# Optimization experiments

Hardware: AMD Instinct MI355X
Metric: run time of the kernel (lower is better)

Reference implementation:

```python
import jax, jax.numpy as jnp
import numpy as np

_BLOCK = 32          # _QUANTIZATION_BLOCK_SIZE
_UPPER = 8           # upper_bound = 2**(4-1)-1 + 1 for Q4_0 (bitwidth=4)
_QMAX = 15.0         # 2**bitwidth - 1


def _q4_0_dequant(kernel):
    """Vectorized Q4_0 fake-quantization over 32-element blocks (last axis, no transpose)."""
    orig_dtype = kernel.dtype
    nb = kernel.size // _BLOCK
    blocks = kernel.reshape(nb, _BLOCK).astype(jnp.float32)  # [nb, 32]
    # signed value at the abs-argmax position of each block
    amax_idx = jnp.argmax(jnp.abs(blocks), axis=1)
    max_val = jnp.take_along_axis(blocks, amax_idx[:, None], axis=1)  # [nb, 1]
    d = -max_val / _UPPER
    safe_d = jnp.where(d == 0.0, 1.0, d)
    safe_inv_d = jnp.where(d == 0.0, 0.0, 1.0 / safe_d)
    scale = d.astype(jnp.float16).astype(jnp.float32)  # fp16 scale round-trip
    qs = jnp.clip(jnp.trunc(blocks * safe_inv_d + (_UPPER + 0.5)), 0.0, _QMAX)
    deq = scale * (qs - _UPPER)
    return deq.reshape(kernel.shape).astype(orig_dtype)


def _ste_q4_0(kernel):
    """Straight-through estimator wrapper (identity gradient)."""
    zero = kernel - jax.lax.stop_gradient(kernel)
    return zero + jax.lax.stop_gradient(_q4_0_dequant(kernel))


def setup_inputs() -> dict:
    key = jax.random.key(0)
    k1, k2, k3 = jax.random.split(key, 3)
    d_in, features = 8192, 8192
    inputs = jax.random.normal(k1, (1, 32, d_in), dtype=jnp.float32)
    kernel = jax.random.normal(k2, (d_in, features), dtype=jnp.float32) * 0.02
    bias = jax.random.normal(k3, (features,), dtype=jnp.float32) * 0.02
    return {"inputs": inputs, "kernel": kernel, "bias": bias}


def reference(inputs, kernel, bias):
    w = _ste_q4_0(kernel)                      # fake-quantized weight [d_in, features]
    y = inputs @ w                             # [B, S, features]
    y = y + bias
    return y
```

## Files before the change

### kernel.cpp

```cpp
#include <hip/hip_runtime.h>
#include <hip/hip_fp16.h>

#define MDIM 32
#define KDIM 8192
#define NDIM 8192
#define NT 128
#define KC 512
#define BK 64
#define NTILES (KC / BK)
#define WSTRIDE 72

typedef __fp16 half8 __attribute__((ext_vector_type(8)));
typedef float f32x4 __attribute__((ext_vector_type(4)));

__device__ __forceinline__ unsigned pk_u32(float a, float b) {
#if __has_builtin(__builtin_amdgcn_cvt_pkrtz)
  return __builtin_bit_cast(unsigned, __builtin_amdgcn_cvt_pkrtz(a, b));
#else
  __fp16 r2[2] = {(__fp16)a, (__fp16)b};
  return __builtin_bit_cast(unsigned, r2);
#endif
}

__global__ __launch_bounds__(256) void xpack_kernel(const float* __restrict__ x,
                                                    uint4* __restrict__ xpf) {
  const int T  = blockIdx.x * 256 + threadIdx.x;
  const int sg = T >> 7;
  const int r  = T & 127;
  const int mt = r >> 6;
  const int L  = r & 63;
  const int m  = mt * 16 + (L & 15);
  const int k  = sg * 32 + (L >> 4) * 8;
  const float4* p = reinterpret_cast<const float4*>(x + (size_t)m * KDIM + k);
  float4 u0 = p[0], u1 = p[1];
  uint4 o;
  o.x = pk_u32(u0.x, u0.y);
  o.y = pk_u32(u0.z, u0.w);
  o.z = pk_u32(u1.x, u1.y);
  o.w = pk_u32(u1.z, u1.w);
  xpf[T] = o;
}

__global__ __launch_bounds__(256, 4) void fused_q4_gemm(
    const uint4* __restrict__ xpf,
    const float* __restrict__ w,
    const float* __restrict__ bias,
    float* __restrict__ out)
{
  __shared__ _Float16 s_w[NT * WSTRIDE];

  const int t  = threadIdx.x;
  const int n0 = blockIdx.x * NT;
  const int k0 = blockIdx.y * KC;

  const int kr = t >> 3;
  const int nc = t & 7;

  const int lane = t & 63;
  const int wv   = t >> 6;
  const int l15  = lane & 15;
  const int q    = lane >> 4;

  f32x4 acc00 = {0.f, 0.f, 0.f, 0.f};
  f32x4 acc01 = {0.f, 0.f, 0.f, 0.f};
  f32x4 acc10 = {0.f, 0.f, 0.f, 0.f};
  f32x4 acc11 = {0.f, 0.f, 0.f, 0.f};

  unsigned* sw32 = reinterpret_cast<unsigned*>(s_w);

  for (int tt = 0; tt < NTILES; ++tt) {
    const int kt = k0 + tt * BK;

    {
      const float* rp = w + (size_t)(kt + 2 * kr) * NDIM + n0 + nc * 16;
      float4 v0[4], v1[4];
#pragma unroll
      for (int j = 0; j < 4; ++j) {
        v0[j] = reinterpret_cast<const float4*>(rp)[j];
        v1[j] = reinterpret_cast<const float4*>(rp + NDIM)[j];
      }
      float ba0 = -1.0f, bv0 = 0.0f, ba1 = -1.0f, bv1 = 0.0f;
#pragma unroll
      for (int j = 0; j < 4; ++j) {
        float c, a;
        c = v0[j].x; a = fabsf(c); if (a > ba0) { ba0 = a; bv0 = c; }
        c = v0[j].y; a = fabsf(c); if (a > ba0) { ba0 = a; bv0 = c; }
        c = v0[j].z; a = fabsf(c); if (a > ba0) { ba0 = a; bv0 = c; }
        c = v0[j].w; a = fabsf(c); if (a > ba0) { ba0 = a; bv0 = c; }
        c = v1[j].x; a = fabsf(c); if (a > ba1) { ba1 = a; bv1 = c; }
        c = v1[j].y; a = fabsf(c); if (a > ba1) { ba1 = a; bv1 = c; }
        c = v1[j].z; a = fabsf(c); if (a > ba1) { ba1 = a; bv1 = c; }
        c = v1[j].w; a = fabsf(c); if (a > ba1) { ba1 = a; bv1 = c; }
      }
      float pa0 = __shfl_xor(ba0, 1), pv0 = __shfl_xor(bv0, 1);
      float pa1 = __shfl_xor(ba1, 1), pv1 = __shfl_xor(bv1, 1);
      const bool odd = (t & 1);
      if (odd ? (pa0 >= ba0) : (pa0 > ba0)) bv0 = pv0;
      if (odd ? (pa1 >= ba1) : (pa1 > ba1)) bv1 = pv1;

      float d0 = bv0 * -0.125f;
      float i0 = (d0 == 0.0f) ? 0.0f : 1.0f / d0;
      float s0 = __half2float(__float2half(d0));
      float d1 = bv1 * -0.125f;
      float i1 = (d1 == 0.0f) ? 0.0f : 1.0f / d1;
      float s1 = __half2float(__float2half(d1));

      unsigned pw[16];
#pragma unroll
      for (int j = 0; j < 4; ++j) {
        float qv, a0f, a1f;
#define DQ(comp, idx)                                                        \
        qv = fminf(fmaxf(truncf(fmaf(v0[j].comp, i0, 8.5f)), 0.0f), 15.0f);  \
        a0f = (qv - 8.0f) * s0;                                              \
        qv = fminf(fmaxf(truncf(fmaf(v1[j].comp, i1, 8.5f)), 0.0f), 15.0f);  \
        a1f = (qv - 8.0f) * s1;                                              \
        pw[j * 4 + idx] = pk_u32(a0f, a1f);
        DQ(x, 0) DQ(y, 1) DQ(z, 2) DQ(w, 3)
#undef DQ
      }
#pragma unroll
      for (int i = 0; i < 16; ++i) {
        const int n = nc * 16 + i;
        sw32[n * (WSTRIDE / 2) + kr] = pw[i];
      }
    }

    __syncthreads();

    const int sgbase = kt >> 5;
#pragma unroll
    for (int ks = 0; ks < 2; ++ks) {
      const uint4* ap = xpf + ((size_t)(sgbase + ks) * 2) * 64 + lane;
      uint4 a0u = ap[0];
      uint4 a1u = ap[64];
      const int kl = ks * 32 + q * 8;
      uint4 b0u = *reinterpret_cast<const uint4*>(&s_w[(wv * 32 + l15) * WSTRIDE + kl]);
      uint4 b1u = *reinterpret_cast<const uint4*>(&s_w[(wv * 32 + 16 + l15) * WSTRIDE + kl]);
      half8 a0 = __builtin_bit_cast(half8, a0u);
      half8 a1 = __builtin_bit_cast(half8, a1u);
      half8 b0 = __builtin_bit_cast(half8, b0u);
      half8 b1 = __builtin_bit_cast(half8, b1u);
      acc00 = __builtin_amdgcn_mfma_f32_16x16x32_f16(a0, b0, acc00, 0, 0, 0);
      acc01 = __builtin_amdgcn_mfma_f32_16x16x32_f16(a0, b1, acc01, 0, 0, 0);
      acc10 = __builtin_amdgcn_mfma_f32_16x16x32_f16(a1, b0, acc10, 0, 0, 0);
      acc11 = __builtin_amdgcn_mfma_f32_16x16x32_f16(a1, b1, acc11, 0, 0, 0);
    }
    __syncthreads();
  }

  const int gn0 = n0 + wv * 32 + l15;
  const int gn1 = gn0 + 16;
  const float bv0 = (blockIdx.y == 0) ? bias[gn0] : 0.0f;
  const float bv1 = (blockIdx.y == 0) ? bias[gn1] : 0.0f;
#pragma unroll
  for (int r = 0; r < 4; ++r) {
    const int m0 = q * 4 + r;
    const int m1 = 16 + q * 4 + r;
    atomicAdd(out + (size_t)m0 * NDIM + gn0, acc00[r] + bv0);
    atomicAdd(out + (size_t)m0 * NDIM + gn1, acc01[r] + bv1);
    atomicAdd(out + (size_t)m1 * NDIM + gn0, acc10[r] + bv0);
    atomicAdd(out + (size_t)m1 * NDIM + gn1, acc11[r] + bv1);
  }
}

extern "C" void kernel_launch(void* const* d_in, const int* in_sizes, int n_in,
                              void* d_out, int out_size, void* d_ws, size_t ws_size,
                              hipStream_t stream) {
  const float* x    = (const float*)d_in[0];
  const float* w    = (const float*)d_in[1];
  const float* bias = (const float*)d_in[2];
  float* out  = (float*)d_out;
  uint4* xpf  = (uint4*)d_ws;

  (void)hipMemsetAsync(out, 0, (size_t)MDIM * NDIM * sizeof(float), stream);
  xpack_kernel<<<128, 256, 0, stream>>>(x, xpf);

  dim3 grid(NDIM / NT, KDIM / KC);
  fused_q4_gemm<<<grid, 256, 0, stream>>>(xpf, w, bias, out);
}
```

Measured before the change: 373.4 us.

## Prefetch next weight tile into registers and remap loads for coalescing

Weight loads are restructured so each lane reads one float4 from a row, with 32 lanes covering 128 contiguous columns, making global reads fully coalesced. The 32-element block absmax is now reduced with a three-step xor shuffle across 8 lanes. The next tile's weights are prefetched into registers right after the barrier, so the global loads overlap with the MFMA stage. The shared layout changes to k-pair-major packed half2 words with a padded stride. The trade-off is eight B-operand LDS reads per MFMA pair instead of one vector read, plus extra registers for the prefetch buffer, which may lower occupancy.

```diff
diff --git a/kernel.cpp b/kernel.cpp
--- a/kernel.cpp
+++ b/kernel.cpp
@@ -8,7 +8,8 @@
 #define KC 512
 #define BK 64
 #define NTILES (KC / BK)
-#define WSTRIDE 72
+#define NSPLIT (KDIM / KC)
+#define LSTR 130
 
 typedef __fp16 half8 __attribute__((ext_vector_type(8)));
 typedef float f32x4 __attribute__((ext_vector_type(4)));
@@ -47,95 +48,100 @@
     const float* __restrict__ bias,
     float* __restrict__ out)
 {
-  __shared__ _Float16 s_w[NT * WSTRIDE];
+  __shared__ unsigned sW[32 * LSTR];
 
-  const int t  = threadIdx.x;
-  const int n0 = blockIdx.x * NT;
-  const int k0 = blockIdx.y * KC;
-
-  const int kr = t >> 3;
-  const int nc = t & 7;
-
+  const int t    = threadIdx.x;
+  const int n0   = blockIdx.x * NT;
+  const int k0   = blockIdx.y * KC;
   const int lane = t & 63;
   const int wv   = t >> 6;
   const int l15  = lane & 15;
   const int q    = lane >> 4;
+  const int h    = lane >> 5;
+  const int nl   = (lane & 31) * 4;
 
   f32x4 acc00 = {0.f, 0.f, 0.f, 0.f};
   f32x4 acc01 = {0.f, 0.f, 0.f, 0.f};
   f32x4 acc10 = {0.f, 0.f, 0.f, 0.f};
   f32x4 acc11 = {0.f, 0.f, 0.f, 0.f};
 
-  unsigned* sw32 = reinterpret_cast<unsigned*>(s_w);
+  float4 V[8];
+
+#pragma unroll
+  for (int p = 0; p < 8; ++p) {
+    const int sp = p * 4 + wv;
+    V[p] = *reinterpret_cast<const float4*>(
+        w + (size_t)(k0 + 2 * sp + h) * NDIM + n0 + nl);
+  }
 
   for (int tt = 0; tt < NTILES; ++tt) {
     const int kt = k0 + tt * BK;
 
-    {
-      const float* rp = w + (size_t)(kt + 2 * kr) * NDIM + n0 + nc * 16;
-      float4 v0[4], v1[4];
 #pragma unroll
-      for (int j = 0; j < 4; ++j) {
-        v0[j] = reinterpret_cast<const float4*>(rp)[j];
-        v1[j] = reinterpret_cast<const float4*>(rp + NDIM)[j];
+    for (int p = 0; p < 8; ++p) {
+      const int sp = p * 4 + wv;
+      float4 v = V[p];
+      float ba = -1.0f, bv = 0.0f, a;
+      a = fabsf(v.x); if (a > ba) { ba = a; bv = v.x; }
+      a = fabsf(v.y); if (a > ba) { ba = a; bv = v.y; }
+      a = fabsf(v.z); if (a > ba) { ba = a; bv = v.z; }
+      a = fabsf(v.w); if (a > ba) { ba = a; bv = v.w; }
+#pragma unroll
+      for (int msk = 1; msk <= 4; msk <<= 1) {
+        float pa = __shfl_xor(ba, msk);
+        float pv = __shfl_xor(bv, msk);
+        if (pa > ba) { ba = pa; bv = pv; }
       }
-      float ba0 = -1.0f, bv0 = 0.0f, ba1 = -1.0f, bv1 = 0.0f;
-#pragma unroll
-      for (int j = 0; j < 4; ++j) {
-        float c, a;
-        c = v0[j].x; a = fabsf(c); if (a > ba0) { ba0 = a; bv0 = c; }
-        c = v0[j].y; a = fabsf(c); if (a > ba0) { ba0 = a; bv0 = c; }
-        c = v0[j].z; a = fabsf(c); if (a > ba0) { ba0 = a; bv0 = c; }
-        c = v0[j].w; a = fabsf(c); if (a > ba0) { ba0 = a; bv0 = c; }
-        c = v1[j].x; a = fabsf(c); if (a > ba1) { ba1 = a; bv1 = c; }
-        c = v1[j].y; a = fabsf(c); if (a > ba1) { ba1 = a; bv1 = c; }
-        c = v1[j].z; a = fabsf(c); if (a > ba1) { ba1 = a; bv1 = c; }
-        c = v1[j].w; a = fabsf(c); if (a > ba1) { ba1 = a; bv1 = c; }
-      }
-      float pa0 = __shfl_xor(ba0, 1), pv0 = __shfl_xor(bv0, 1);
-      float pa1 = __shfl_xor(ba1, 1), pv1 = __shfl_xor(bv1, 1);
-      const bool odd = (t & 1);
-      if (odd ? (pa0 >= ba0) : (pa0 > ba0)) bv0 = pv0;
-      if (odd ? (pa1 >= ba1) : (pa1 > ba1)) bv1 = pv1;
-
-      float d0 = bv0 * -0.125f;
-      float i0 = (d0 == 0.0f) ? 0.0f : 1.0f / d0;
-      float s0 = __half2float(__float2half(d0));
-      float d1 = bv1 * -0.125f;
-      float i1 = (d1 == 0.0f) ? 0.0f : 1.0f / d1;
-      float s1 = __half2float(__float2half(d1));
-
-      unsigned pw[16];
-#pragma unroll
-      for (int j = 0; j < 4; ++j) {
-        float qv, a0f, a1f;
-#define DQ(comp, idx)                                                        \
-        qv = fminf(fmaxf(truncf(fmaf(v0[j].comp, i0, 8.5f)), 0.0f), 15.0f);  \
-        a0f = (qv - 8.0f) * s0;                                              \
-        qv = fminf(fmaxf(truncf(fmaf(v1[j].comp, i1, 8.5f)), 0.0f), 15.0f);  \
-        a1f = (qv - 8.0f) * s1;                                              \
-        pw[j * 4 + idx] = pk_u32(a0f, a1f);
-        DQ(x, 0) DQ(y, 1) DQ(z, 2) DQ(w, 3)
-#undef DQ
-      }
-#pragma unroll
-      for (int i = 0; i < 16; ++i) {
-        const int n = nc * 16 + i;
-        sw32[n * (WSTRIDE / 2) + kr] = pw[i];
-      }
+      float d   = bv * -0.125f;
+      float inv = (d == 0.0f) ? 0.0f : 1.0f / d;
+      float s   = __half2float(__float2half(d));
+      float q0f = fminf(fmaxf(truncf(fmaf(v.x, inv, 8.5f)), 0.0f), 15.0f);
+      float q1f = fminf(fmaxf(truncf(fmaf(v.y, inv, 8.5f)), 0.0f), 15.0f);
+      float q2f = fminf(fmaxf(truncf(fmaf(v.z, inv, 8.5f)), 0.0f), 15.0f);
+      float q3f = fminf(fmaxf(truncf(fmaf(v.w, inv, 8.5f)), 0.0f), 15.0f);
+      unsigned A = pk_u32((q0f - 8.0f) * s, (q1f - 8.0f) * s);
+      unsigned B = pk_u32((q2f - 8.0f) * s, (q3f - 8.0f) * s);
+      unsigned pA = (unsigned)__shfl_xor((int)A, 32);
+      unsigned pB = (unsigned)__shfl_xor((int)B, 32);
+      unsigned lo0 = h ? pA : A, hi0 = h ? A : pA;
+      unsigned lo1 = h ? pB : B, hi1 = h ? B : pB;
+      unsigned D0 = (lo0 & 0xffffu) | (hi0 << 16);
+      unsigned D1 = (lo0 >> 16)     | (hi0 & 0xffff0000u);
+      unsigned D2 = (lo1 & 0xffffu) | (hi1 << 16);
+      unsigned D3 = (lo1 >> 16)     | (hi1 & 0xffff0000u);
+      uint2 wr = h ? make_uint2(D2, D3) : make_uint2(D0, D1);
+      *reinterpret_cast<uint2*>(&sW[sp * LSTR + nl + 2 * h]) = wr;
     }
 
     __syncthreads();
 
-    const int sgbase = kt >> 5;
+    if (tt + 1 < NTILES) {
+#pragma unroll
+      for (int p = 0; p < 8; ++p) {
+        const int sp = p * 4 + wv;
+        V[p] = *reinterpret_cast<const float4*>(
+            w + (size_t)(kt + BK + 2 * sp + h) * NDIM + n0 + nl);
+      }
+    }
+
+    const int sg0 = kt >> 5;
 #pragma unroll
     for (int ks = 0; ks < 2; ++ks) {
-      const uint4* ap = xpf + ((size_t)(sgbase + ks) * 2) * 64 + lane;
+      const uint4* ap = xpf + ((size_t)(sg0 + ks) * 2) * 64 + lane;
       uint4 a0u = ap[0];
       uint4 a1u = ap[64];
-      const int kl = ks * 32 + q * 8;
-      uint4 b0u = *reinterpret_cast<const uint4*>(&s_w[(wv * 32 + l15) * WSTRIDE + kl]);
-      uint4 b1u = *reinterpret_cast<const uint4*>(&s_w[(wv * 32 + 16 + l15) * WSTRIDE + kl]);
+      const int kpb = ks * 16 + q * 4;
+      const int nA = wv * 32 + l15;
+      const int nB = nA + 16;
+      uint4 b0u, b1u;
+      b0u.x = sW[(kpb + 0) * LSTR + nA];
+      b0u.y = sW[(kpb + 1) * LSTR + nA];
+      b0u.z = sW[(kpb + 2) * LSTR + nA];
+      b0u.w = sW[(kpb + 3) * LSTR + nA];
+      b1u.x = sW[(kpb + 0) * LSTR + nB];
+      b1u.y = sW[(kpb + 1) * LSTR + nB];
+      b1u.z = sW[(kpb + 2) * LSTR + nB];
+      b1u.w = sW[(kpb + 3) * LSTR + nB];
       half8 a0 = __builtin_bit_cast(half8, a0u);
       half8 a1 = __builtin_bit_cast(half8, a1u);
       half8 b0 = __builtin_bit_cast(half8, b0u);
@@ -145,6 +151,7 @@
       acc10 = __builtin_amdgcn_mfma_f32_16x16x32_f16(a1, b0, acc10, 0, 0, 0);
       acc11 = __builtin_amdgcn_mfma_f32_16x16x32_f16(a1, b1, acc11, 0, 0, 0);
     }
+
     __syncthreads();
   }
 
@@ -155,7 +162,7 @@
 #pragma unroll
   for (int r = 0; r < 4; ++r) {
     const int m0 = q * 4 + r;
-    const int m1 = 16 + q * 4 + r;
+    const int m1 = m0 + 16;
     atomicAdd(out + (size_t)m0 * NDIM + gn0, acc00[r] + bv0);
     atomicAdd(out + (size_t)m0 * NDIM + gn1, acc01[r] + bv1);
     atomicAdd(out + (size_t)m1 * NDIM + gn0, acc10[r] + bv0);
@@ -175,6 +182,6 @@
   (void)hipMemsetAsync(out, 0, (size_t)MDIM * NDIM * sizeof(float), stream);
   xpack_kernel<<<128, 256, 0, stream>>>(x, xpf);
 
-  dim3 grid(NDIM / NT, KDIM / KC);
+  dim3 grid(NDIM / NT, NSPLIT);
   fused_q4_gemm<<<grid, 256, 0, stream>>>(xpf, w, bias, out);
 }
```

After: 362.3 us. 3.0% less time.
